# Kernel optimization log

Hardware: AMD Instinct MI355X
Metric: run time of the kernel (lower is better)

The kernel has to match this reference:

```python
import jax, jax.numpy as jnp
import numpy as np

NUM_HEADS = 16
LN_EPS = 1e-5


def _layer_norm(x, g, b):
    m = x.mean(-1, keepdims=True)
    v = x.var(-1, keepdims=True)
    return (x - m) / jnp.sqrt(v + LN_EPS) * g + b


def setup_inputs() -> dict:
    key = jax.random.key(0)
    ks = jax.random.split(key, 4)
    Bq, Bk, Nk, C = 128, 128, 256, 1024
    return {
        "qx": jax.random.normal(ks[0], (Bq, 1, C), jnp.float32),
        "kx": jax.random.normal(ks[1], (Bk, Nk, C), jnp.float32),
        "gq": jnp.ones((C,), jnp.float32),
        "bq": jnp.zeros((C,), jnp.float32),
        "gk": jnp.ones((C,), jnp.float32),
        "bk": jnp.zeros((C,), jnp.float32),
        "Wq": jax.random.normal(ks[2], (C, C), jnp.float32) * (C ** -0.5),
        "Wk": jax.random.normal(ks[3], (C, C), jnp.float32) * (C ** -0.5),
    }


def reference(qx, kx, gq, bq, gk, bk, Wq, Wk):
    H = NUM_HEADS
    Bq, _, C = qx.shape  # qx: [Bq, 1, C]
    Bk, Nk, _ = kx.shape  # kx: [Bk, Nk, C]
    hd = C // H
    scale = hd ** -0.5
    # LayerNorm + linear projections (nn.Linear: x @ W.T, no bias)
    q = (_layer_norm(qx, gq, bq) @ Wq.T).reshape(Bq, H, hd)       # [Bq, H, hd] (Nq=1 squeezed)
    k = (_layer_norm(kx, gk, bk) @ Wk.T).reshape(Bk, Nk, H, hd)   # [Bk, Nk, H, hd]
    # Full bipartite cross-batch attention scores: [Bq, Bk, H, Nk]
    attn = jnp.einsum('qhc,knhc->qkhn', q, k) * scale
    attn = jax.nn.softmax(attn, axis=-1)
    # v = kx broadcast over heads in original einsum 'khnc,qkhn->qkc';
    # equivalent: sum attn over heads, then contract over Nk.
    w = attn.sum(axis=2)                                           # [Bq, Bk, Nk]
    x = jnp.einsum('knc,qkn->qkc', kx, w)                          # [Bq, Bk, C]
    return x
```

## Files before the change

kernel.cpp:

```cpp
#include <hip/hip_runtime.h>


typedef unsigned short ushort_t;
typedef __bf16 bf16x8 __attribute__((ext_vector_type(8)));
typedef float f32x4 __attribute__((ext_vector_type(4)));

#define AS1 __attribute__((address_space(1)))
#define AS3 __attribute__((address_space(3)))

__device__ __forceinline__ void gload_lds16(const void* g, void* l) {
  __builtin_amdgcn_global_load_lds((const AS1 unsigned int*)g, (AS3 unsigned int*)l, 16, 0, 0);
}

__device__ __forceinline__ ushort_t f2bf(float f) {
  unsigned u = __float_as_uint(f);
  unsigned r = u + 0x7FFFu + ((u >> 16) & 1u);
  return (ushort_t)(r >> 16);
}

__global__ __launch_bounds__(256) void cvt_bf16_kernel(const float* __restrict__ src,
                                                       ushort_t* __restrict__ dst, int n4) {
  int i = blockIdx.x * 256 + threadIdx.x;
  if (i < n4) {
    float4 v = ((const float4*)src)[i];
    ushort4 o;
    o.x = f2bf(v.x); o.y = f2bf(v.y); o.z = f2bf(v.z); o.w = f2bf(v.w);
    ((ushort4*)dst)[i] = o;
  }
}

__global__ __launch_bounds__(256) void ln_kernel(const float* __restrict__ kx,
                                                 const float* __restrict__ qx,
                                                 const float* __restrict__ gk,
                                                 const float* __restrict__ bk,
                                                 const float* __restrict__ gq,
                                                 const float* __restrict__ bq,
                                                 ushort_t* __restrict__ kln,
                                                 ushort_t* __restrict__ qln) {
  const int tid = threadIdx.x, lane = tid & 63, wid = tid >> 6;

  const float* src; ushort_t* dst; const float* gp; const float* bp;
  if (blockIdx.x < 8192) {
    const int row = blockIdx.x * 4 + wid;
    src = kx + (size_t)row * 1024; dst = kln + (size_t)row * 1024; gp = gk; bp = bk;
  } else {
    const int row = (blockIdx.x - 8192) * 4 + wid;
    src = qx + (size_t)row * 1024; dst = qln + (size_t)row * 1024; gp = gq; bp = bq;
  }
  const int c0 = lane * 4;

  float4 v0 = *(const float4*)(src + c0);
  float4 v1 = *(const float4*)(src + c0 + 256);
  float4 v2 = *(const float4*)(src + c0 + 512);
  float4 v3 = *(const float4*)(src + c0 + 768);

  float s  = (v0.x + v0.y + v0.z + v0.w) + (v1.x + v1.y + v1.z + v1.w)
           + (v2.x + v2.y + v2.z + v2.w) + (v3.x + v3.y + v3.z + v3.w);
  float s2 = (v0.x*v0.x + v0.y*v0.y + v0.z*v0.z + v0.w*v0.w)
           + (v1.x*v1.x + v1.y*v1.y + v1.z*v1.z + v1.w*v1.w)
           + (v2.x*v2.x + v2.y*v2.y + v2.z*v2.z + v2.w*v2.w)
           + (v3.x*v3.x + v3.y*v3.y + v3.z*v3.z + v3.w*v3.w);
  #pragma unroll
  for (int off = 1; off < 64; off <<= 1) {
    s  += __shfl_xor(s, off);
    s2 += __shfl_xor(s2, off);
  }
  const float mean = s * (1.0f / 1024.0f);
  const float var  = s2 * (1.0f / 1024.0f) - mean * mean;
  const float rstd = rsqrtf(var + 1e-5f);

  float4 g0 = *(const float4*)(gp + c0);
  float4 g1 = *(const float4*)(gp + c0 + 256);
  float4 g2 = *(const float4*)(gp + c0 + 512);
  float4 g3 = *(const float4*)(gp + c0 + 768);
  float4 b0 = *(const float4*)(bp + c0);
  float4 b1 = *(const float4*)(bp + c0 + 256);
  float4 b2 = *(const float4*)(bp + c0 + 512);
  float4 b3 = *(const float4*)(bp + c0 + 768);

  ushort4 o0, o1, o2, o3;
  o0.x = f2bf((v0.x - mean) * rstd * g0.x + b0.x);
  o0.y = f2bf((v0.y - mean) * rstd * g0.y + b0.y);
  o0.z = f2bf((v0.z - mean) * rstd * g0.z + b0.z);
  o0.w = f2bf((v0.w - mean) * rstd * g0.w + b0.w);
  o1.x = f2bf((v1.x - mean) * rstd * g1.x + b1.x);
  o1.y = f2bf((v1.y - mean) * rstd * g1.y + b1.y);
  o1.z = f2bf((v1.z - mean) * rstd * g1.z + b1.z);
  o1.w = f2bf((v1.w - mean) * rstd * g1.w + b1.w);
  o2.x = f2bf((v2.x - mean) * rstd * g2.x + b2.x);
  o2.y = f2bf((v2.y - mean) * rstd * g2.y + b2.y);
  o2.z = f2bf((v2.z - mean) * rstd * g2.z + b2.z);
  o2.w = f2bf((v2.w - mean) * rstd * g2.w + b2.w);
  o3.x = f2bf((v3.x - mean) * rstd * g3.x + b3.x);
  o3.y = f2bf((v3.y - mean) * rstd * g3.y + b3.y);
  o3.z = f2bf((v3.z - mean) * rstd * g3.z + b3.z);
  o3.w = f2bf((v3.w - mean) * rstd * g3.w + b3.w);

  *(ushort4*)(dst + c0)       = o0;
  *(ushort4*)(dst + c0 + 256) = o1;
  *(ushort4*)(dst + c0 + 512) = o2;
  *(ushort4*)(dst + c0 + 768) = o3;
}

__global__ __launch_bounds__(512, 2) void gemm256_kernel(const ushort_t* __restrict__ A,
                                                         const ushort_t* __restrict__ Bt,
                                                         ushort_t* __restrict__ Cpk,
                                                         const ushort_t* __restrict__ qA,
                                                         const ushort_t* __restrict__ qB,
                                                         ushort_t* __restrict__ qC,
                                                         int M, int N) {
  __shared__ ushort_t Abuf[3][16384];
  __shared__ ushort_t Bbuf[2][16384];

  const int tid = threadIdx.x, lane = tid & 63, wid = tid >> 6;
  const int g = lane >> 4, rr = lane & 15;
  const int wr = wid >> 2, wc = wid & 3;

  const int Mt = M >> 8, Nt = N >> 8;
  const int nwg = Mt * Nt;
  const int qq = nwg >> 3, r8 = nwg & 7;
  const int xcd = blockIdx.x & 7, idx = blockIdx.x >> 3;
  const int wg = (xcd < r8 ? xcd * (qq + 1) : r8 * (qq + 1) + (xcd - r8) * qq) + idx;
  const int mt = wg / Nt, nt = wg - mt * Nt;
  const size_t m0 = (size_t)mt << 8, n0 = (size_t)nt << 8;

  const ushort_t* Abase = A  + m0 * 1024;
  const ushort_t* Bbase = Bt + n0 * 1024;

  f32x4 acc[8][4];
  #pragma unroll
  for (int i = 0; i < 8; ++i)
    #pragma unroll
    for (int j = 0; j < 4; ++j) acc[i][j] = (f32x4){0.f, 0.f, 0.f, 0.f};

  auto stA = [&](int kt) {
    ushort_t* dst = &Abuf[kt % 3][0];
    #pragma unroll
    for (int l = 0; l < 4; ++l) {
      int ix = l * 512 + tid;
      int r  = ix >> 3;
      int gs = (ix & 7) ^ (((r >> 2) & 1) << 1);
      gload_lds16(Abase + (size_t)r * 1024 + (kt << 6) + (gs << 3), dst + ix * 8);
    }
  };
  auto stB = [&](int kt) {
    ushort_t* dst = &Bbuf[kt & 1][0];
    #pragma unroll
    for (int l = 0; l < 4; ++l) {
      int ix = l * 512 + tid;
      int r  = ix >> 3;
      int gs = (ix & 7) ^ (((r >> 2) & 1) << 1);
      gload_lds16(Bbase + (size_t)r * 1024 + (kt << 6) + (gs << 3), dst + ix * 8);
    }
  };

  stA(0); stB(0); stA(1);
  asm volatile("s_waitcnt vmcnt(4)" ::: "memory");
  __builtin_amdgcn_s_barrier();

  const int sw = ((rr >> 2) & 1) << 1;

  #pragma unroll 1
  for (int j = 0; j < 16; ++j) {
    const ushort_t* as = &Abuf[j % 3][0];
    const ushort_t* bs = &Bbuf[j & 1][0];

    {
      bf16x8 af[8], bf[4];
      #pragma unroll
      for (int i = 0; i < 8; ++i) {
        int r = (wr << 7) + (i << 4) + rr;
        af[i] = *(const bf16x8*)&as[(r << 6) + ((g ^ sw) << 3)];
      }
      #pragma unroll
      for (int jj = 0; jj < 4; ++jj) {
        int r = (wc << 6) + (jj << 4) + rr;
        bf[jj] = *(const bf16x8*)&bs[(r << 6) + ((g ^ sw) << 3)];
      }
      if (j < 15) stB(j + 1);
      if (j < 14) stA(j + 2);
      __builtin_amdgcn_s_setprio(1);
      #pragma unroll
      for (int i = 0; i < 8; ++i)
        #pragma unroll
        for (int jj = 0; jj < 4; ++jj)
          acc[i][jj] = __builtin_amdgcn_mfma_f32_16x16x32_bf16(af[i], bf[jj], acc[i][jj], 0, 0, 0);
      __builtin_amdgcn_s_setprio(0);
    }
    {
      bf16x8 af[8], bf[4];
      #pragma unroll
      for (int i = 0; i < 8; ++i) {
        int r = (wr << 7) + (i << 4) + rr;
        af[i] = *(const bf16x8*)&as[(r << 6) + (((4 + g) ^ sw) << 3)];
      }
      #pragma unroll
      for (int jj = 0; jj < 4; ++jj) {
        int r = (wc << 6) + (jj << 4) + rr;
        bf[jj] = *(const bf16x8*)&bs[(r << 6) + (((4 + g) ^ sw) << 3)];
      }
      __builtin_amdgcn_s_setprio(1);
      #pragma unroll
      for (int i = 0; i < 8; ++i)
        #pragma unroll
        for (int jj = 0; jj < 4; ++jj)
          acc[i][jj] = __builtin_amdgcn_mfma_f32_16x16x32_bf16(af[i], bf[jj], acc[i][jj], 0, 0, 0);
      __builtin_amdgcn_s_setprio(0);
      if (j < 14) {
        asm volatile("s_waitcnt vmcnt(4)" ::: "memory");
        __builtin_amdgcn_s_barrier();
      } else if (j == 14) {
        asm volatile("s_waitcnt vmcnt(0)" ::: "memory");
        __builtin_amdgcn_s_barrier();
      }
    }
  }

  #pragma unroll
  for (int i = 0; i < 8; ++i)
    #pragma unroll
    for (int j = 0; j < 4; ++j)
      #pragma unroll
      for (int rg = 0; rg < 4; ++rg) {
        size_t row = m0 + (wr << 7) + (i << 4) + (g << 2) + rg;
        size_t col = n0 + (wc << 6) + (j << 4) + rr;
        int kb = (int)(row >> 8), t = (int)((row >> 4) & 15), r16 = (int)(row & 15);
        int h = (int)(col >> 6), ch = (int)(col & 63);
        size_t odx = ((((size_t)kb * 16 + h) * 16 + t) << 10)
                   + ((ch >> 5) << 9) + (((ch >> 3) & 3) << 7) + (r16 << 3) + (ch & 7);
        Cpk[odx] = f2bf(acc[i][j][rg]);
      }

  if ((wg & 63) < 8) {
    const int ti = ((wg >> 6) << 6) + ((wg & 7) << 3) + wid;
    const int mq = ti >> 6, nq = ti & 63;
    const ushort_t* qa = qA + (size_t)(mq * 16 + rr) * 1024 + g * 8;
    const ushort_t* qb = qB + (size_t)(nq * 16 + rr) * 1024 + g * 8;
    f32x4 qacc0 = (f32x4){0.f, 0.f, 0.f, 0.f};
    f32x4 qacc1 = (f32x4){0.f, 0.f, 0.f, 0.f};
    #pragma unroll
    for (int kk = 0; kk < 32; kk += 2) {
      bf16x8 a0 = *(const bf16x8*)(qa + kk * 32);
      bf16x8 b0 = *(const bf16x8*)(qb + kk * 32);
      bf16x8 a1 = *(const bf16x8*)(qa + kk * 32 + 32);
      bf16x8 b1 = *(const bf16x8*)(qb + kk * 32 + 32);
      qacc0 = __builtin_amdgcn_mfma_f32_16x16x32_bf16(a0, b0, qacc0, 0, 0, 0);
      qacc1 = __builtin_amdgcn_mfma_f32_16x16x32_bf16(a1, b1, qacc1, 0, 0, 0);
    }
    #pragma unroll
    for (int rg = 0; rg < 4; ++rg)
      qC[(size_t)(mq * 16 + (g << 2) + rg) * 1024 + nq * 16 + rr] = f2bf(qacc0[rg] + qacc1[rg]);
  }
}

__global__ __launch_bounds__(256, 3) void scores_kernel(const ushort_t* __restrict__ qp,
                                                        const ushort_t* __restrict__ kpk,
                                                        ushort_t* __restrict__ wbuf) {
  __shared__ float pbuf[2][16][258];

  const int tid = threadIdx.x, lane = tid & 63, wid = tid >> 6;
  const int g = lane >> 4, rr = lane & 15;

  const int b = blockIdx.x;
  const int wg = (b & 7) * 128 + (b >> 3);
  const int kb = wg >> 3;
  const int q0 = (wg & 7) << 4;

  const int hs = wid;

  float w_acc[16][4];
  #pragma unroll
  for (int t = 0; t < 16; ++t)
    #pragma unroll
    for (int r = 0; r < 4; ++r) w_acc[t][r] = 0.f;

  const ushort_t* qrow = qp + (size_t)(q0 + rr) * 1024;
  const ushort_t* kbb  = kpk + ((size_t)kb * 16) * 16384 + g * 128 + rr * 8;

  for (int hp = 0; hp < 4; ++hp) {
    const int h = hp * 4 + hs;
    const int co = h * 64 + g * 8;
    bf16x8 aq0 = *(const bf16x8*)(qrow + co);
    bf16x8 aq1 = *(const bf16x8*)(qrow + co + 32);
    const ushort_t* hb = kbb + (size_t)h * 16384;
    f32x4 s[16];
    #pragma unroll
    for (int t = 0; t < 16; ++t) {
      bf16x8 b0 = *(const bf16x8*)(hb + t * 1024);
      bf16x8 b1 = *(const bf16x8*)(hb + t * 1024 + 512);
      f32x4 a = (f32x4){0.f, 0.f, 0.f, 0.f};
      a = __builtin_amdgcn_mfma_f32_16x16x32_bf16(aq0, b0, a, 0, 0, 0);
      a = __builtin_amdgcn_mfma_f32_16x16x32_bf16(aq1, b1, a, 0, 0, 0);
      s[t] = a;
    }
    #pragma unroll
    for (int r = 0; r < 4; ++r) {
      float mx = s[0][r];
      #pragma unroll
      for (int t = 1; t < 16; ++t) mx = fmaxf(mx, s[t][r]);
      mx = fmaxf(mx, __shfl_xor(mx, 1));
      mx = fmaxf(mx, __shfl_xor(mx, 2));
      mx = fmaxf(mx, __shfl_xor(mx, 4));
      mx = fmaxf(mx, __shfl_xor(mx, 8));
      float sum = 0.f;
      float e[16];
      #pragma unroll
      for (int t = 0; t < 16; ++t) {
        e[t] = __expf((s[t][r] - mx) * 0.125f);
        sum += e[t];
      }
      sum += __shfl_xor(sum, 1);
      sum += __shfl_xor(sum, 2);
      sum += __shfl_xor(sum, 4);
      sum += __shfl_xor(sum, 8);
      float inv = 1.0f / sum;
      #pragma unroll
      for (int t = 0; t < 16; ++t) w_acc[t][r] += e[t] * inv;
    }
  }

  __syncthreads();
  if (hs >= 2) {
    #pragma unroll
    for (int t = 0; t < 16; ++t)
      #pragma unroll
      for (int r = 0; r < 4; ++r)
        pbuf[hs - 2][(g << 2) + r][t * 16 + rr] = w_acc[t][r];
  }
  __syncthreads();
  if (hs < 2) {
    #pragma unroll
    for (int t = 0; t < 16; ++t)
      #pragma unroll
      for (int r = 0; r < 4; ++r)
        w_acc[t][r] += pbuf[hs][(g << 2) + r][t * 16 + rr];
    if (hs == 1) {
      #pragma unroll
      for (int t = 0; t < 16; ++t)
        #pragma unroll
        for (int r = 0; r < 4; ++r)
          pbuf[1][(g << 2) + r][t * 16 + rr] = w_acc[t][r];
    }
  }
  __syncthreads();
  if (hs == 0) {
    ushort_t* wb = wbuf + (size_t)kb * 32768;
    #pragma unroll
    for (int t = 0; t < 16; ++t)
      #pragma unroll
      for (int r = 0; r < 4; ++r) {
        float v = w_acc[t][r] + pbuf[1][(g << 2) + r][t * 16 + rr];
        wb[(size_t)(q0 + (g << 2) + r) * 256 + t * 16 + rr] = f2bf(v);
      }
  }
}

__global__ __launch_bounds__(256, 4) void pv_kernel(const ushort_t* __restrict__ wbuf,
                                                    const float* __restrict__ kx,
                                                    float* __restrict__ xout) {
  const int tid = threadIdx.x, lane = tid & 63, wid = tid >> 6;
  const int g = lane >> 4, rr = lane & 15;

  const int b = blockIdx.x;
  const int wg = (b & 7) * 128 + (b >> 3);
  const int kb = wg >> 3;
  const int c0 = (wg & 7) * 128;

  const int wr = wid >> 1, wc = wid & 1;

  f32x4 acc[4][4];
  #pragma unroll
  for (int i = 0; i < 4; ++i)
    #pragma unroll
    for (int j = 0; j < 4; ++j) acc[i][j] = (f32x4){0.f, 0.f, 0.f, 0.f};

  const ushort_t* wb = wbuf + (size_t)kb * 32768;
  const float* kxb = kx + (size_t)kb * 256 * 1024;

  for (int nc = 0; nc < 8; ++nc) {
    const int n0 = nc * 32 + g * 8;
    bf16x8 af[4];
    #pragma unroll
    for (int i = 0; i < 4; ++i) {
      int q = (wr << 6) + (i << 4) + rr;
      af[i] = *(const bf16x8*)(wb + (size_t)q * 256 + n0);
    }
    #pragma unroll
    for (int j = 0; j < 4; ++j) {
      int c = c0 + (wc << 6) + (j << 4) + rr;
      const float* src = kxb + (size_t)n0 * 1024 + c;
      float f[8];
      #pragma unroll
      for (int jj = 0; jj < 8; ++jj) f[jj] = src[(size_t)jj * 1024];
      bf16x8 bb;
      #pragma unroll
      for (int jj = 0; jj < 8; ++jj) bb[jj] = (__bf16)f[jj];
      #pragma unroll
      for (int i = 0; i < 4; ++i)
        acc[i][j] = __builtin_amdgcn_mfma_f32_16x16x32_bf16(af[i], bb, acc[i][j], 0, 0, 0);
    }
  }

  #pragma unroll
  for (int i = 0; i < 4; ++i)
    #pragma unroll
    for (int j = 0; j < 4; ++j)
      #pragma unroll
      for (int rg = 0; rg < 4; ++rg) {
        int q = (wr << 6) + (i << 4) + (g << 2) + rg;
        int c = c0 + (wc << 6) + (j << 4) + rr;
        xout[((size_t)q * 128 + kb) * 1024 + c] = acc[i][j][rg];
      }
}

extern "C" void kernel_launch(void* const* d_in, const int* in_sizes, int n_in,
                              void* d_out, int out_size, void* d_ws, size_t ws_size,
                              hipStream_t stream) {
  const float* qx = (const float*)d_in[0];
  const float* kx = (const float*)d_in[1];
  const float* gq = (const float*)d_in[2];
  const float* bq = (const float*)d_in[3];
  const float* gk = (const float*)d_in[4];
  const float* bk = (const float*)d_in[5];
  const float* Wq = (const float*)d_in[6];
  const float* Wk = (const float*)d_in[7];

  char* ws = (char*)d_ws;
  ushort_t* kkp   = (ushort_t*)(ws);
  ushort_t* qproj = (ushort_t*)(ws + 67108864);
  ushort_t* wbuf  = (ushort_t*)(ws + 67371008);
  ushort_t* qln   = (ushort_t*)(ws + 67371008);
  ushort_t* Wqb   = (ushort_t*)(ws + 67371008 + 262144);
  ushort_t* Wkb   = (ushort_t*)(ws + 67371008 + 2359296);
  ushort_t* kln  = (ushort_t*)d_out;
  float*    xout = (float*)d_out;

  cvt_bf16_kernel<<<1024, 256, 0, stream>>>(Wq, Wqb, 262144);
  cvt_bf16_kernel<<<1024, 256, 0, stream>>>(Wk, Wkb, 262144);
  ln_kernel<<<8192 + 32, 256, 0, stream>>>(kx, qx, gk, bk, gq, bq, kln, qln);
  gemm256_kernel<<<512, 512, 0, stream>>>(kln, Wkb, kkp, qln, Wqb, qproj, 32768, 1024);
  scores_kernel<<<1024, 256, 0, stream>>>(qproj, kkp, wbuf);
  pv_kernel<<<1024, 256, 0, stream>>>(wbuf, kx, xout);
}
```

Before: 258.8 us.

## Split GEMM k-step into four barrier-separated MFMA phases with staggered prefetch

Restructures the main K-loop of the bf16 projection GEMM into four sub-phases, each loading a subset of B fragments from LDS and issuing 16 MFMAs, with barriers between phases and the B/A global-to-LDS prefetches issued in different phases. The aim is to interleave LDS reads, async global loads and MFMA work more finely, as in 8-wave ping-pong style schedules, and to cut register pressure from holding all B fragments. It adds extra workgroup barriers per iteration, which could add synchronization stalls.

```diff
diff --git a/kernel.cpp b/kernel.cpp
--- a/kernel.cpp
+++ b/kernel.cpp
@@ -164,55 +164,80 @@
   for (int j = 0; j < 16; ++j) {
     const ushort_t* as = &Abuf[j % 3][0];
     const ushort_t* bs = &Bbuf[j & 1][0];
-
-    {
-      bf16x8 af[8], bf[4];
-      #pragma unroll
-      for (int i = 0; i < 8; ++i) {
-        int r = (wr << 7) + (i << 4) + rr;
-        af[i] = *(const bf16x8*)&as[(r << 6) + ((g ^ sw) << 3)];
-      }
-      #pragma unroll
-      for (int jj = 0; jj < 4; ++jj) {
-        int r = (wc << 6) + (jj << 4) + rr;
-        bf[jj] = *(const bf16x8*)&bs[(r << 6) + ((g ^ sw) << 3)];
-      }
-      if (j < 15) stB(j + 1);
-      if (j < 14) stA(j + 2);
-      __builtin_amdgcn_s_setprio(1);
-      #pragma unroll
-      for (int i = 0; i < 8; ++i)
-        #pragma unroll
-        for (int jj = 0; jj < 4; ++jj)
-          acc[i][jj] = __builtin_amdgcn_mfma_f32_16x16x32_bf16(af[i], bf[jj], acc[i][jj], 0, 0, 0);
-      __builtin_amdgcn_s_setprio(0);
-    }
-    {
-      bf16x8 af[8], bf[4];
-      #pragma unroll
-      for (int i = 0; i < 8; ++i) {
-        int r = (wr << 7) + (i << 4) + rr;
-        af[i] = *(const bf16x8*)&as[(r << 6) + (((4 + g) ^ sw) << 3)];
-      }
-      #pragma unroll
-      for (int jj = 0; jj < 4; ++jj) {
-        int r = (wc << 6) + (jj << 4) + rr;
-        bf[jj] = *(const bf16x8*)&bs[(r << 6) + (((4 + g) ^ sw) << 3)];
-      }
-      __builtin_amdgcn_s_setprio(1);
-      #pragma unroll
-      for (int i = 0; i < 8; ++i)
-        #pragma unroll
-        for (int jj = 0; jj < 4; ++jj)
-          acc[i][jj] = __builtin_amdgcn_mfma_f32_16x16x32_bf16(af[i], bf[jj], acc[i][jj], 0, 0, 0);
-      __builtin_amdgcn_s_setprio(0);
-      if (j < 14) {
-        asm volatile("s_waitcnt vmcnt(4)" ::: "memory");
-        __builtin_amdgcn_s_barrier();
-      } else if (j == 14) {
-        asm volatile("s_waitcnt vmcnt(0)" ::: "memory");
-        __builtin_amdgcn_s_barrier();
-      }
+    bf16x8 af[8], b01[2], b23[2];
+
+    #pragma unroll
+    for (int i = 0; i < 8; ++i) {
+      int r = (wr << 7) + (i << 4) + rr;
+      af[i] = *(const bf16x8*)&as[(r << 6) + ((g ^ sw) << 3)];
+    }
+    #pragma unroll
+    for (int jj = 0; jj < 2; ++jj) {
+      int r = (wc << 6) + (jj << 4) + rr;
+      b01[jj] = *(const bf16x8*)&bs[(r << 6) + ((g ^ sw) << 3)];
+    }
+    if (j < 15) stB(j + 1);
+    __builtin_amdgcn_s_setprio(1);
+    #pragma unroll
+    for (int i = 0; i < 8; ++i) {
+      acc[i][0] = __builtin_amdgcn_mfma_f32_16x16x32_bf16(af[i], b01[0], acc[i][0], 0, 0, 0);
+      acc[i][1] = __builtin_amdgcn_mfma_f32_16x16x32_bf16(af[i], b01[1], acc[i][1], 0, 0, 0);
+    }
+    __builtin_amdgcn_s_setprio(0);
+    __builtin_amdgcn_s_barrier();
+
+    #pragma unroll
+    for (int jj = 0; jj < 2; ++jj) {
+      int r = (wc << 6) + ((jj + 2) << 4) + rr;
+      b23[jj] = *(const bf16x8*)&bs[(r << 6) + ((g ^ sw) << 3)];
+    }
+    if (j < 14) stA(j + 2);
+    __builtin_amdgcn_s_setprio(1);
+    #pragma unroll
+    for (int i = 0; i < 8; ++i) {
+      acc[i][2] = __builtin_amdgcn_mfma_f32_16x16x32_bf16(af[i], b23[0], acc[i][2], 0, 0, 0);
+      acc[i][3] = __builtin_amdgcn_mfma_f32_16x16x32_bf16(af[i], b23[1], acc[i][3], 0, 0, 0);
+    }
+    __builtin_amdgcn_s_setprio(0);
+    __builtin_amdgcn_s_barrier();
+
+    #pragma unroll
+    for (int i = 0; i < 8; ++i) {
+      int r = (wr << 7) + (i << 4) + rr;
+      af[i] = *(const bf16x8*)&as[(r << 6) + (((4 + g) ^ sw) << 3)];
+    }
+    #pragma unroll
+    for (int jj = 0; jj < 2; ++jj) {
+      int r = (wc << 6) + (jj << 4) + rr;
+      b01[jj] = *(const bf16x8*)&bs[(r << 6) + (((4 + g) ^ sw) << 3)];
+    }
+    __builtin_amdgcn_s_setprio(1);
+    #pragma unroll
+    for (int i = 0; i < 8; ++i) {
+      acc[i][0] = __builtin_amdgcn_mfma_f32_16x16x32_bf16(af[i], b01[0], acc[i][0], 0, 0, 0);
+      acc[i][1] = __builtin_amdgcn_mfma_f32_16x16x32_bf16(af[i], b01[1], acc[i][1], 0, 0, 0);
+    }
+    __builtin_amdgcn_s_setprio(0);
+    __builtin_amdgcn_s_barrier();
+
+    #pragma unroll
+    for (int jj = 0; jj < 2; ++jj) {
+      int r = (wc << 6) + ((jj + 2) << 4) + rr;
+      b23[jj] = *(const bf16x8*)&bs[(r << 6) + (((4 + g) ^ sw) << 3)];
+    }
+    __builtin_amdgcn_s_setprio(1);
+    #pragma unroll
+    for (int i = 0; i < 8; ++i) {
+      acc[i][2] = __builtin_amdgcn_mfma_f32_16x16x32_bf16(af[i], b23[0], acc[i][2], 0, 0, 0);
+      acc[i][3] = __builtin_amdgcn_mfma_f32_16x16x32_bf16(af[i], b23[1], acc[i][3], 0, 0, 0);
+    }
+    __builtin_amdgcn_s_setprio(0);
+    if (j < 14) {
+      asm volatile("s_waitcnt vmcnt(4)" ::: "memory");
+      __builtin_amdgcn_s_barrier();
+    } else if (j == 14) {
+      asm volatile("s_waitcnt vmcnt(0)" ::: "memory");
+      __builtin_amdgcn_s_barrier();
     }
   }
 
```

Measured after the change: 265.2 us. 2.4% more time.
